# Kernel optimization log

Hardware: AMD Instinct MI355X
Metric: run time of the kernel (lower is better)

Reference implementation:

```python
import jax, jax.numpy as jnp
import numpy as np

S, B, T = 16, 32, 64        # max_sents, batch, max_tokens
V, E, H = 50000, 256, 256   # vocab, embed_size, gru_hidden (n_dim)
NC = 50                     # n_classes


def setup_inputs() -> dict:
    key = jax.random.key(0)
    ks = jax.random.split(key, 30)

    def u(k, shape, s=0.1):
        return jax.random.uniform(k, shape, minval=-s, maxval=s, dtype=jnp.float32)

    return {
        "x": jax.random.randint(ks[0], (S, B, T), 0, V, dtype=jnp.int64),
        "embed": jax.random.normal(ks[1], (V, E), dtype=jnp.float32) * 0.1,
        # word-level bi-GRU (input E, hidden H); gate order r,z,n as in torch
        "wg_Wih_f": u(ks[2], (3 * H, E)), "wg_Whh_f": u(ks[3], (3 * H, H)),
        "wg_bih_f": u(ks[4], (3 * H,)),   "wg_bhh_f": u(ks[5], (3 * H,)),
        "wg_Wih_b": u(ks[6], (3 * H, E)), "wg_Whh_b": u(ks[7], (3 * H, H)),
        "wg_bih_b": u(ks[8], (3 * H,)),   "wg_bhh_b": u(ks[9], (3 * H,)),
        "word_W": u(ks[10], (2 * H, 2 * H)),
        "word_b": u(ks[11], (2 * H, 1)),
        "word_proj": u(ks[12], (2 * H, 1)),
        # sentence-level bi-GRU (input 2H, hidden H)
        "sg_Wih_f": u(ks[13], (3 * H, 2 * H)), "sg_Whh_f": u(ks[14], (3 * H, H)),
        "sg_bih_f": u(ks[15], (3 * H,)),       "sg_bhh_f": u(ks[16], (3 * H,)),
        "sg_Wih_b": u(ks[17], (3 * H, 2 * H)), "sg_Whh_b": u(ks[18], (3 * H, H)),
        "sg_bih_b": u(ks[19], (3 * H,)),       "sg_bhh_b": u(ks[20], (3 * H,)),
        "sent_W": u(ks[21], (2 * H, 2 * H)),
        "sent_b": u(ks[22], (2 * H, 1)),
        "sent_proj": u(ks[23], (2 * H, 1)),
        "fin_W": u(ks[24], (NC, 2 * H)),
        "fin_b": u(ks[25], (NC,)),
        "state_word": jnp.zeros((2, B, H), dtype=jnp.float32),
        "state_sent": jnp.zeros((2, B, H), dtype=jnp.float32),
    }


def _gru_dir(x, h0, Wih, Whh, bih, bhh, reverse=False):
    # x: [T, B, in]; returns hidden states [T, B, H] (in original time order)
    xp = jnp.einsum('tbe,ge->tbg', x, Wih) + bih  # precompute input projections

    def step(h, xt):
        g = h @ Whh.T + bhh
        xr, xz, xn = jnp.split(xt, 3, axis=-1)
        hr, hz, hn = jnp.split(g, 3, axis=-1)
        r = jax.nn.sigmoid(xr + hr)
        z = jax.nn.sigmoid(xz + hz)
        n = jnp.tanh(xn + r * hn)
        h = (1.0 - z) * n + z * h
        return h, h

    _, hs = jax.lax.scan(step, h0, xp, reverse=reverse)
    return hs


def _bigru(x, h0, Wf, Hf, bif, bhf, Wb, Hb, bib, bhb):
    f = _gru_dir(x, h0[0], Wf, Hf, bif, bhf, reverse=False)
    b = _gru_dir(x, h0[1], Wb, Hb, bib, bhb, reverse=True)
    return jnp.concatenate([f, b], axis=-1)  # [T, B, 2H]


def _attn_pool(out, W, b, proj):
    # out: [T, B, 2H]; batch_matmul_bias(tanh) -> batch_matmul -> softmax over T -> weighted sum
    squish = jnp.tanh(jnp.einsum('tbh,hk->tbk', out, W) + b[:, 0])  # [T,B,2H]
    scores = jnp.einsum('tbk,k->tb', squish, proj[:, 0])            # [T,B]
    a = jax.nn.softmax(scores, axis=0)                              # softmax over seq
    return jnp.einsum('tb,tbh->bh', a, out)                         # [B,2H]


def reference(x, embed,
              wg_Wih_f, wg_Whh_f, wg_bih_f, wg_bhh_f,
              wg_Wih_b, wg_Whh_b, wg_bih_b, wg_bhh_b,
              word_W, word_b, word_proj,
              sg_Wih_f, sg_Whh_f, sg_bih_f, sg_bhh_f,
              sg_Wih_b, sg_Whh_b, sg_bih_b, sg_bhh_b,
              sent_W, sent_b, sent_proj,
              fin_W, fin_b, state_word, state_sent):
    e = embed[x]                         # [S,B,T,E]
    e = jnp.transpose(e, (0, 2, 1, 3))   # [S,T,B,E] (torch code transposes per sentence)

    word_out = jax.vmap(
        lambda xs: _bigru(xs, state_word,
                          wg_Wih_f, wg_Whh_f, wg_bih_f, wg_bhh_f,
                          wg_Wih_b, wg_Whh_b, wg_bih_b, wg_bhh_b)
    )(e)                                 # [S,T,B,2H]

    s = jax.vmap(lambda o: _attn_pool(o, word_W, word_b, word_proj))(word_out)  # [S,B,2H]

    sent_out = _bigru(s, state_sent,
                      sg_Wih_f, sg_Whh_f, sg_bih_f, sg_bhh_f,
                      sg_Wih_b, sg_Whh_b, sg_bih_b, sg_bhh_b)  # [S,B,2H]
    pooled = _attn_pool(sent_out, sent_W, sent_b, sent_proj)   # [B,2H]
    return pooled @ fin_W.T + fin_b                            # [B,NC] logits
```

## Files before the change

### kernel.cpp

```cpp
#include <hip/hip_runtime.h>


typedef float  f32x4  __attribute__((ext_vector_type(4)));
typedef int    i32x4  __attribute__((ext_vector_type(4)));
typedef __bf16 bf16x8 __attribute__((ext_vector_type(8)));

#define DEVINL static __device__ __forceinline__

DEVINL unsigned short f2bf(float f) {
    __bf16 b = (__bf16)f;
    return __builtin_bit_cast(unsigned short, b);
}
DEVINL float bf2f(unsigned short u) {
    unsigned int x = ((unsigned int)u) << 16;
    return __builtin_bit_cast(float, x);
}
DEVINL float bfe16(unsigned int v, int hi) {
    return bf2f((unsigned short)(hi ? (v >> 16) : (v & 0xffffu)));
}
DEVINL float sigm(float x) { return __builtin_amdgcn_rcpf(1.f + __expf(-x)); }
DEVINL float tanh_(float x) {
    x = fminf(fmaxf(x, -20.f), 20.f);
    float e = __expf(-2.f * x);
    return (1.f - e) * __builtin_amdgcn_rcpf(1.f + e);
}
DEVINL void mfma16(f32x4& acc, i32x4 a, i32x4 b) {
    acc = __builtin_amdgcn_mfma_f32_16x16x32_bf16(
        __builtin_bit_cast(bf16x8, a), __builtin_bit_cast(bf16x8, b), acc, 0, 0, 0);
}
DEVINL f32x4 zero4() { f32x4 v = {0.f, 0.f, 0.f, 0.f}; return v; }
DEVINL i32x4 pack8f(f32x4 v0, f32x4 v1) {
    i32x4 p;
    p.x = (int)((unsigned)f2bf(v0.x) | ((unsigned)f2bf(v0.y) << 16));
    p.y = (int)((unsigned)f2bf(v0.z) | ((unsigned)f2bf(v0.w) << 16));
    p.z = (int)((unsigned)f2bf(v1.x) | ((unsigned)f2bf(v1.y) << 16));
    p.w = (int)((unsigned)f2bf(v1.z) | ((unsigned)f2bf(v1.w) << 16));
    return p;
}

#define O_WPWF    ((size_t)0)
#define O_WPWB    ((size_t)1048576)
#define O_WPSGIH  ((size_t)2097152)
#define O_WPSHHF  ((size_t)3670016)
#define O_WPSHHB  ((size_t)4063232)
#define O_WPWW    ((size_t)4456448)
#define O_WPSW    ((size_t)4980736)
#define O_BIASWF  ((size_t)5505024)
#define O_BIASWB  ((size_t)5509120)
#define O_BIHCAT  ((size_t)5513216)
#define O_WOUT    ((size_t)5519360)
#define O_SCORESW ((size_t)39073792)
#define O_SSFRAG  ((size_t)39204864)
#define O_XPSENT  ((size_t)39729152)
#define O_SOFRAG  ((size_t)42874880)
#define O_SCORESS ((size_t)43399168)
#define WS_NEED_B ((size_t)43401216)
#define O_XPW     ((size_t)43401216)
#define WS_NEED_A ((size_t)144064512)

__global__ void k_prep(const float* wihf, const float* whhf,
                       const float* wihb, const float* whhb,
                       const float* sgihf, const float* sgihb,
                       const float* sghhf, const float* sghhb,
                       const float* wordW, const float* sentW,
                       const float* bihf, const float* bhhf,
                       const float* bihb, const float* bhhb,
                       const float* sgbihf, const float* sgbihb,
                       const float* sgbhhf, const float* sgbhhb,
                       unsigned short* Wpwf, unsigned short* Wpwb,
                       unsigned short* Wpsgih,
                       unsigned short* WpshhF, unsigned short* WpshhB,
                       unsigned short* WpwW, unsigned short* WpsW,
                       float* biasWf, float* biasWb, float* bihCat)
{
    const int tid0 = blockIdx.x * blockDim.x + threadIdx.x;
    const int nth  = gridDim.x * blockDim.x;

    for (int c = tid0; c < 2 * 65536; c += nth) {
        int d = c >> 16, chunk = c & 65535;
        int lane = chunk & 63, nk = chunk >> 6;
        int kf = nk & 15, nf = nk >> 4;
        int n = nf * 16 + (lane & 15);
        int k0 = kf * 32 + (lane >> 4) * 8;
        int g4 = n >> 8, jj = n & 255;
        i32x4 p = {0, 0, 0, 0};
        const bool zero = (k0 < 256) ? (g4 == 3) : (g4 == 2);
        if (!zero) {
            const float* src;
            if (k0 < 256) {
                src = (d ? wihb : wihf) + (g4 * 256 + jj) * 256 + k0;
            } else {
                int row = (g4 == 3) ? (512 + jj) : (g4 * 256 + jj);
                src = (d ? whhb : whhf) + row * 256 + (k0 - 256);
            }
            p = pack8f(*(const f32x4*)src, *(const f32x4*)(src + 4));
        }
        *(i32x4*)((d ? Wpwb : Wpwf) + chunk * 8) = p;
    }
    for (int chunk = tid0; chunk < 98304; chunk += nth) {
        int lane = chunk & 63, nk = chunk >> 6;
        int kf = nk & 15, nf = nk >> 4;
        int n = nf * 16 + (lane & 15);
        int k0 = kf * 32 + (lane >> 4) * 8;
        const float* src = (n < 768) ? sgihf + n * 512 + k0
                                     : sgihb + (n - 768) * 512 + k0;
        *(i32x4*)(Wpsgih + chunk * 8) =
            pack8f(*(const f32x4*)src, *(const f32x4*)(src + 4));
    }
    for (int c = tid0; c < 2 * 24576; c += nth) {
        int d = c >= 24576, chunk = d ? c - 24576 : c;
        int lane = chunk & 63, nk = chunk >> 6;
        int kf = nk & 7, nf = nk >> 3;
        int n = nf * 16 + (lane & 15);
        int k0 = kf * 32 + (lane >> 4) * 8;
        const float* src = (d ? sghhb : sghhf) + n * 256 + k0;
        *(i32x4*)((d ? WpshhB : WpshhF) + chunk * 8) =
            pack8f(*(const f32x4*)src, *(const f32x4*)(src + 4));
    }
    for (int c = tid0; c < 2 * 32768; c += nth) {
        int d = c >> 15, chunk = c & 32767;
        int lane = chunk & 63, nk = chunk >> 6;
        int kf = nk & 15, nf = nk >> 4;
        int n = nf * 16 + (lane & 15);
        int k0 = kf * 32 + (lane >> 4) * 8;
        const float* W = (d ? sentW : wordW) + (size_t)k0 * 512 + n;
        unsigned short us[8];
#pragma unroll
        for (int j = 0; j < 8; ++j) us[j] = f2bf(W[j * 512]);
        i32x4 p;
        p.x = (int)((unsigned)us[0] | ((unsigned)us[1] << 16));
        p.y = (int)((unsigned)us[2] | ((unsigned)us[3] << 16));
        p.z = (int)((unsigned)us[4] | ((unsigned)us[5] << 16));
        p.w = (int)((unsigned)us[6] | ((unsigned)us[7] << 16));
        *(i32x4*)((d ? WpsW : WpwW) + chunk * 8) = p;
    }
    for (int idx = tid0; idx < 2048; idx += nth) {
        int d = idx >> 10, i = idx & 1023;
        int g4 = i >> 8, j = i & 255;
        const float* bi = d ? bihb : bihf;
        const float* bh = d ? bhhb : bhhf;
        float v = (g4 == 0) ? bi[j] + bh[j]
                : (g4 == 1) ? bi[256 + j] + bh[256 + j]
                : (g4 == 2) ? bi[512 + j] : bh[512 + j];
        (d ? biasWb : biasWf)[i] = v;
    }
    for (int idx = tid0; idx < 1536; idx += nth) {
        int d = idx >= 768, j = d ? idx - 768 : idx;
        const float* bi = d ? sgbihb : sgbihf;
        const float* bh = d ? sgbhhb : sgbhhf;
        bihCat[idx] = bi[j] + ((j < 512) ? bh[j] : 0.f);
    }
}

__global__ __launch_bounds__(512, 2)
void k_xpw(const int* xg, const float* embed,
           const unsigned short* Wpwf_u, const unsigned short* Wpwb_u,
           const float* biasWf, const float* biasWb, unsigned short* xpw)
{
    __shared__ unsigned short Ebuf[2][16][256];
    const int tid = threadIdx.x, lane = tid & 63, w = tid >> 6;
    const int cid = blockIdx.x;
    const int tq = cid & 3, bh = (cid >> 2) & 1, dir = (cid >> 3) & 1, s = cid >> 4;
    const int t0 = tq * 16;
    const i32x4* Wp = (const i32x4*)(dir ? Wpwb_u : Wpwf_u);
    const float* biasW = dir ? biasWb : biasWf;
    const int b = lane & 15, rsub = lane >> 4;

    i32x4 A[3][2][8];
#pragma unroll
    for (int g = 0; g < 3; ++g)
#pragma unroll
        for (int q = 0; q < 2; ++q)
#pragma unroll
            for (int kk = 0; kk < 8; ++kk)
                A[g][q][kk] = Wp[((g * 16 + w * 2 + q) * 16 + kk) * 64 + lane];

    unsigned int biasp[3][2][2];
#pragma unroll
    for (int g = 0; g < 3; ++g)
#pragma unroll
        for (int q = 0; q < 2; ++q) {
            const int j0 = g * 256 + (w * 2 + q) * 16 + rsub * 4;
            biasp[g][q][0] = (unsigned)f2bf(biasW[j0]) |
                             ((unsigned)f2bf(biasW[j0 + 1]) << 16);
            biasp[g][q][1] = (unsigned)f2bf(biasW[j0 + 2]) |
                             ((unsigned)f2bf(biasW[j0 + 3]) << 16);
        }

    const int sb = tid >> 5, sc = tid & 31;
    const int tokrow = (s * 32 + bh * 16 + sb) * 64;
    const int sdst = sb * 512 + ((sc * 16) ^ ((sb & 7) << 4));

#define STAGE_E(BUF, T)                                                       \
    {                                                                         \
        const int tok = xg[tokrow + (T)];                                     \
        const f32x4* src = (const f32x4*)(embed + (size_t)tok * 256 + sc * 8);\
        *(i32x4*)((char*)&Ebuf[BUF][0][0] + sdst) = pack8f(src[0], src[1]);   \
    }

    STAGE_E(0, t0);
    const size_t chain = (size_t)((s * 2 + dir) * 2 + bh);
    char* const xpBase = (char*)xpw + chain * 1572864 +
                         (size_t)(rsub * 128 + b * 8);

    for (int tl = 0; tl < 16; ++tl) {
        __syncthreads();
        const int t = t0 + tl, cur = tl & 1, nxt = cur ^ 1;
        if (tl < 15) STAGE_E(nxt, t + 1);

        f32x4 acc[3][2];
#pragma unroll
        for (int g = 0; g < 3; ++g) { acc[g][0] = zero4(); acc[g][1] = zero4(); }
#pragma unroll
        for (int kk = 0; kk < 8; ++kk) {
            const int roff = b * 512 + ((kk * 64 + rsub * 16) ^ ((b & 7) << 4));
            i32x4 eb = *(const i32x4*)((const char*)&Ebuf[cur][0][0] + roff);
            mfma16(acc[0][0], A[0][0][kk], eb); mfma16(acc[0][1], A[0][1][kk], eb);
            mfma16(acc[1][0], A[1][0][kk], eb); mfma16(acc[1][1], A[1][1][kk], eb);
            mfma16(acc[2][0], A[2][0][kk], eb); mfma16(acc[2][1], A[2][1][kk], eb);
        }
        char* ob = xpBase + (size_t)t * 24576;
#pragma unroll
        for (int g = 0; g < 3; ++g)
#pragma unroll
            for (int q = 0; q < 2; ++q) {
                unsigned short us[4];
#pragma unroll
                for (int i = 0; i < 4; ++i)
                    us[i] = f2bf(acc[g][q][i] + bfe16(biasp[g][q][i >> 1], i & 1));
                uint2 pk;
                pk.x = (unsigned)us[0] | ((unsigned)us[1] << 16);
                pk.y = (unsigned)us[2] | ((unsigned)us[3] << 16);
                *(uint2*)(ob + g * 8192 + (w * 2 + q) * 512) = pk;
            }
    }
#undef STAGE_E
}

__global__ __launch_bounds__(512, 2)
void k_gru_wordA(const float* stateW,
                 const unsigned short* Wpwf_u, const unsigned short* Wpwb_u,
                 const float* biasWf, const float* biasWb,
                 const unsigned short* xpw, unsigned short* wout)
{
    __shared__ unsigned short Hbuf[2][16][256];
    const int tid = threadIdx.x, lane = tid & 63, w = tid >> 6;
    const int cid = blockIdx.x, bh = cid & 1, dir = (cid >> 1) & 1, s = cid >> 2;
    const i32x4* Wp = (const i32x4*)(dir ? Wpwb_u : Wpwf_u);
    const float* biasW = dir ? biasWb : biasWf;
    const int b = lane & 15, rsub = lane >> 4;
    const int gmap[3] = {0, 1, 3};

    i32x4 A[3][2][8];
#pragma unroll
    for (int g = 0; g < 3; ++g)
#pragma unroll
        for (int q = 0; q < 2; ++q)
#pragma unroll
            for (int kk = 0; kk < 8; ++kk)
                A[g][q][kk] =
                    Wp[((gmap[g] * 16 + w * 2 + q) * 16 + 8 + kk) * 64 + lane];

    unsigned int bhnp[2][2];
    float hreg[2][4];
#pragma unroll
    for (int q = 0; q < 2; ++q) {
        const int j0 = (w * 2 + q) * 16 + rsub * 4;
        f32x4 h0 = *(const f32x4*)(stateW + dir * 8192 + (bh * 16 + b) * 256 + j0);
        bhnp[q][0] = (unsigned)f2bf(biasW[768 + j0]) |
                     ((unsigned)f2bf(biasW[768 + j0 + 1]) << 16);
        bhnp[q][1] = (unsigned)f2bf(biasW[768 + j0 + 2]) |
                     ((unsigned)f2bf(biasW[768 + j0 + 3]) << 16);
        hreg[q][0] = h0.x; hreg[q][1] = h0.y; hreg[q][2] = h0.z; hreg[q][3] = h0.w;
        uint2 pk;
        pk.x = (unsigned)f2bf(h0.x) | ((unsigned)f2bf(h0.y) << 16);
        pk.y = (unsigned)f2bf(h0.z) | ((unsigned)f2bf(h0.w) << 16);
        const int boff = b * 512 + (((w * 2 + q) * 32 + rsub * 8) ^ ((b & 7) << 4));
        *(uint2*)((char*)&Hbuf[0][0][0] + boff) = pk;
    }
    const size_t chain = (size_t)((s * 2 + dir) * 2 + bh);
    const char* const xpBase = (const char*)xpw + chain * 1572864 +
                               (size_t)(rsub * 128 + b * 8);

    uint2 xpv[3][2];
    {
        const char* xb = xpBase + (size_t)(dir ? 63 : 0) * 24576;
#pragma unroll
        for (int g = 0; g < 3; ++g)
#pragma unroll
            for (int q = 0; q < 2; ++q)
                xpv[g][q] = *(const uint2*)(xb + g * 8192 + (w * 2 + q) * 512);
    }

    for (int ti = 0; ti < 64; ++ti) {
        __syncthreads();
        const int t = dir ? 63 - ti : ti;
        const int cur = ti & 1, nxt = cur ^ 1;

        uint2 xpn[3][2];
        if (ti < 63) {
            const char* xb = xpBase + (size_t)(dir ? t - 1 : t + 1) * 24576;
#pragma unroll
            for (int g = 0; g < 3; ++g)
#pragma unroll
                for (int q = 0; q < 2; ++q)
                    xpn[g][q] = *(const uint2*)(xb + g * 8192 + (w * 2 + q) * 512);
        }

        f32x4 acc[3][2];
#pragma unroll
        for (int g = 0; g < 3; ++g) { acc[g][0] = zero4(); acc[g][1] = zero4(); }
#pragma unroll
        for (int kk = 0; kk < 8; ++kk) {
            const int roff = b * 512 + ((kk * 64 + rsub * 16) ^ ((b & 7) << 4));
            i32x4 hb = *(const i32x4*)((const char*)&Hbuf[cur][0][0] + roff);
            mfma16(acc[0][0], A[0][0][kk], hb); mfma16(acc[0][1], A[0][1][kk], hb);
            mfma16(acc[1][0], A[1][0][kk], hb); mfma16(acc[1][1], A[1][1][kk], hb);
            mfma16(acc[2][0], A[2][0][kk], hb); mfma16(acc[2][1], A[2][1][kk], hb);
        }
        const int r = (s * 64 + t) * 32 + bh * 16 + b;
#pragma unroll
        for (int q = 0; q < 2; ++q) {
            unsigned short us[4];
#pragma unroll
            for (int i = 0; i < 4; ++i) {
                const unsigned xr = (i < 2) ? xpv[0][q].x : xpv[0][q].y;
                const unsigned xz = (i < 2) ? xpv[1][q].x : xpv[1][q].y;
                const unsigned xn = (i < 2) ? xpv[2][q].x : xpv[2][q].y;
                float rv = sigm(bfe16(xr, i & 1) + acc[0][q][i]);
                float zv = sigm(bfe16(xz, i & 1) + acc[1][q][i]);
                float nv = tanh_(bfe16(xn, i & 1) +
                                 rv * (acc[2][q][i] + bfe16(bhnp[q][i >> 1], i & 1)));
                float h = nv + zv * (hreg[q][i] - nv);
                hreg[q][i] = h;
                us[i] = f2bf(h);
            }
            uint2 pk;
            pk.x = (unsigned)us[0] | ((unsigned)us[1] << 16);
            pk.y = (unsigned)us[2] | ((unsigned)us[3] << 16);
            const int boff = b * 512 + (((w * 2 + q) * 32 + rsub * 8) ^ ((b & 7) << 4));
            *(uint2*)((char*)&Hbuf[nxt][0][0] + boff) = pk;
            const int hcol = dir * 256 + (w * 2 + q) * 16 + rsub * 4;
            const int widx = (((r >> 4) * 16 + (hcol >> 5)) * 64 + (r & 15) +
                              ((hcol >> 3) & 3) * 16) * 8 + (hcol & 7);
            *(uint2*)(wout + widx) = pk;
        }
        if (ti < 63) {
#pragma unroll
            for (int g = 0; g < 3; ++g)
#pragma unroll
                for (int q = 0; q < 2; ++q)
                    xpv[g][q] = xpn[g][q];
        }
    }
}

__global__ __launch_bounds__(1024, 4)
void k_attn_score2(const unsigned short* Afrag_u, const unsigned short* Wp_u,
                   const float* wb, const float* wp, float* scores)
{
    __shared__ i32x4 Wl[2][16][64];
    const int tid = threadIdx.x, lane = tid & 63, w = tid >> 6;
    const int rblk = blockIdx.x * 16 + w;
    const i32x4* A = (const i32x4*)Afrag_u;
    const i32x4* Wg = (const i32x4*)Wp_u;

    i32x4 a[16];
#pragma unroll
    for (int kf = 0; kf < 16; ++kf) a[kf] = A[(rblk * 16 + kf) * 64 + lane];

    i32x4* wl0 = &Wl[0][0][0];
    i32x4* wl1 = &Wl[1][0][0];
    wl0[tid] = Wg[tid];

    float partial[4] = {};
    for (int nf = 0; nf < 32; ++nf) {
        __syncthreads();
        if (nf < 31) {
            i32x4* dst = (nf & 1) ? wl0 : wl1;
            dst[tid] = Wg[(nf + 1) * 1024 + tid];
        }
        const i32x4* cur = (nf & 1) ? wl1 : wl0;
        f32x4 acc0 = zero4(), acc1 = zero4();
#pragma unroll
        for (int kf = 0; kf < 16; kf += 2) {
            mfma16(acc0, a[kf],     cur[kf * 64 + lane]);
            mfma16(acc1, a[kf + 1], cur[(kf + 1) * 64 + lane]);
        }
        const int n = nf * 16 + (lane & 15);
        const float wbn = wb[n], wpn = wp[n];
#pragma unroll
        for (int i = 0; i < 4; ++i)
            partial[i] += tanh_(acc0[i] + acc1[i] + wbn) * wpn;
    }
#pragma unroll
    for (int i = 0; i < 4; ++i) {
        float v = partial[i];
        v += __shfl_xor(v, 1); v += __shfl_xor(v, 2);
        v += __shfl_xor(v, 4); v += __shfl_xor(v, 8);
        if ((lane & 15) == 0)
            scores[rblk * 16 + (lane >> 4) * 4 + i] = v;
    }
}

__global__ void k_attn_score_small(const unsigned short* Afrag_u,
                                   const unsigned short* Wp_u,
                                   const float* wb, const float* wp, float* scores)
{
    const int tid = threadIdx.x, lane = tid & 63, w = tid >> 6;
    const int rblk = blockIdx.x * 4 + w;
    const i32x4* A = (const i32x4*)Afrag_u;
    const i32x4* Wp = (const i32x4*)Wp_u;
    i32x4 a[16];
#pragma unroll
    for (int kf = 0; kf < 16; ++kf) a[kf] = A[(rblk * 16 + kf) * 64 + lane];

    float partial[4] = {};
    for (int nf = 0; nf < 32; ++nf) {
        f32x4 acc0 = zero4(), acc1 = zero4();
#pragma unroll
        for (int kf = 0; kf < 16; kf += 2) {
            mfma16(acc0, a[kf],     Wp[(nf * 16 + kf) * 64 + lane]);
            mfma16(acc1, a[kf + 1], Wp[(nf * 16 + kf + 1) * 64 + lane]);
        }
        const int n = nf * 16 + (lane & 15);
        const float wbn = wb[n], wpn = wp[n];
#pragma unroll
        for (int i = 0; i < 4; ++i)
            partial[i] += tanh_(acc0[i] + acc1[i] + wbn) * wpn;
    }
#pragma unroll
    for (int i = 0; i < 4; ++i) {
        float v = partial[i];
        v += __shfl_xor(v, 1); v += __shfl_xor(v, 2);
        v += __shfl_xor(v, 4); v += __shfl_xor(v, 8);
        if ((lane & 15) == 0)
            scores[rblk * 16 + (lane >> 4) * 4 + i] = v;
    }
}

__global__ void k_word_pool(const float* scores, const unsigned short* wout,
                            unsigned short* ssFrag)
{
    __shared__ float aL[64];
    __shared__ float part[4][64][8];
    const int tid = threadIdx.x, l = tid & 63, w = tid >> 6;
    const int bid = blockIdx.x;
    const int s = bid >> 5, b = bid & 31;
    if (w == 0) {
        float sc = scores[s * 2048 + l * 32 + b];
        float m = sc;
#pragma unroll
        for (int d = 1; d < 64; d <<= 1) m = fmaxf(m, __shfl_xor(m, d));
        float e = __expf(sc - m), sum = e;
#pragma unroll
        for (int d = 1; d < 64; d <<= 1) sum += __shfl_xor(sum, d);
        aL[l] = e * __builtin_amdgcn_rcpf(sum);
    }
    __syncthreads();

    float acc[8] = {};
    const i32x4* WO = (const i32x4*)wout;
    for (int tt = 0; tt < 16; ++tt) {
        const int t = w * 16 + tt;
        float at = aL[t];
        int cidx = ((s * 128 + t * 2 + (b >> 4)) * 16 + (l >> 2)) * 64 +
                   (b & 15) + (l & 3) * 16;
        i32x4 ch = WO[cidx];
        acc[0] += at * bf2f((unsigned short)((unsigned)ch.x & 0xffffu));
        acc[1] += at * bf2f((unsigned short)((unsigned)ch.x >> 16));
        acc[2] += at * bf2f((unsigned short)((unsigned)ch.y & 0xffffu));
        acc[3] += at * bf2f((unsigned short)((unsigned)ch.y >> 16));
        acc[4] += at * bf2f((unsigned short)((unsigned)ch.z & 0xffffu));
        acc[5] += at * bf2f((unsigned short)((unsigned)ch.z >> 16));
        acc[6] += at * bf2f((unsigned short)((unsigned)ch.w & 0xffffu));
        acc[7] += at * bf2f((unsigned short)((unsigned)ch.w >> 16));
    }
#pragma unroll
    for (int q = 0; q < 8; ++q) part[w][l][q] = acc[q];
    __syncthreads();
    if (w == 0) {
        float fin[8];
#pragma unroll
        for (int q = 0; q < 8; ++q)
            fin[q] = part[0][l][q] + part[1][l][q] + part[2][l][q] + part[3][l][q];
        i32x4 pk;
        pk.x = (int)((unsigned)f2bf(fin[0]) | ((unsigned)f2bf(fin[1]) << 16));
        pk.y = (int)((unsigned)f2bf(fin[2]) | ((unsigned)f2bf(fin[3]) << 16));
        pk.z = (int)((unsigned)f2bf(fin[4]) | ((unsigned)f2bf(fin[5]) << 16));
        pk.w = (int)((unsigned)f2bf(fin[6]) | ((unsigned)f2bf(fin[7]) << 16));
        const int r2 = s * 32 + b;
        int cidx2 = ((r2 >> 4) * 16 + (l >> 2)) * 64 + (r2 & 15) + (l & 3) * 16;
        ((i32x4*)ssFrag)[cidx2] = pk;
    }
}

__global__ void k_sgih(const unsigned short* ssFrag_u, const unsigned short* Wp_u,
                       const float* bihCat, float* xpSent)
{
    const int tid = threadIdx.x, lane = tid & 63, w = tid >> 6;
    const int rblk = blockIdx.x, ncl = blockIdx.y;
    const i32x4* A = (const i32x4*)ssFrag_u;
    const i32x4* Wp = (const i32x4*)Wp_u;
    i32x4 a[16];
#pragma unroll
    for (int kf = 0; kf < 16; ++kf) a[kf] = A[(rblk * 16 + kf) * 64 + lane];
#pragma unroll
    for (int nfl = 0; nfl < 4; ++nfl) {
        const int nfg = ncl * 16 + w * 4 + nfl;
        f32x4 acc = zero4();
#pragma unroll
        for (int kf = 0; kf < 16; ++kf)
            mfma16(acc, a[kf], Wp[(nfg * 16 + kf) * 64 + lane]);
        const int n = nfg * 16 + (lane & 15);
        const float bb = bihCat[n];
        const int dir = n >= 768, ng = n - dir * 768;
        const int g = ng >> 8, jj = ng & 255;
#pragma unroll
        for (int i = 0; i < 4; ++i) {
            int row = rblk * 16 + (lane >> 4) * 4 + i;
            int s = row >> 5, b = row & 31;
            xpSent[(((dir * 2 + (b >> 4)) * 16 + s) * 12288) +
                   (g * 256 + jj) * 16 + (b & 15)] = acc[i] + bb;
        }
    }
}

DEVINL void gload16(const void* gsrc, void* ldst) {
    __builtin_amdgcn_global_load_lds(
        (const __attribute__((address_space(1))) unsigned int*)gsrc,
        (__attribute__((address_space(3))) unsigned int*)ldst, 16, 0, 0);
}

__global__ __launch_bounds__(512)
void k_gru_sentA(const float* stateS, const unsigned short* WpF_u,
                 const unsigned short* WpB_u, const float* bhhf, const float* bhhb,
                 const float* xpSent, unsigned short* soFrag)
{
    __shared__ unsigned short Abuf[2][16][256];
    __shared__ float xpLs[2][12288];
    const int tid = threadIdx.x, lane = tid & 63, w = tid >> 6;
    const int cid = blockIdx.x, bh = cid & 1, dir = cid >> 1;
    const i32x4* Wp = (const i32x4*)(dir ? WpB_u : WpF_u);
    const float* bhh = dir ? bhhb : bhhf;

    i32x4 B[3][2][8];
#pragma unroll
    for (int g = 0; g < 3; ++g)
#pragma unroll
        for (int q = 0; q < 2; ++q)
#pragma unroll
            for (int kk = 0; kk < 8; ++kk)
                B[g][q][kk] = Wp[((g * 16 + w * 2 + q) * 8 + kk) * 64 + lane];

    float bhn[2];
    float hreg[2][4];
#pragma unroll
    for (int q = 0; q < 2; ++q) {
        const int j = (w * 2 + q) * 16 + (lane & 15);
        bhn[q] = bhh[512 + j];
#pragma unroll
        for (int i = 0; i < 4; ++i) {
            const int b = 4 * (lane >> 4) + i;
            float h0 = stateS[dir * 8192 + (bh * 16 + b) * 256 + j];
            hreg[q][i] = h0;
            int byteoff = b * 512 + ((j * 2) ^ ((b & 7) << 4));
            *(unsigned short*)((char*)&Abuf[0][0][0] + byteoff) = f2bf(h0);
        }
    }
    const size_t xbase = (size_t)((dir * 2 + bh) * 16) * 49152;
    const int sfirst = dir ? 15 : 0;
#pragma unroll
    for (int c = 0; c < 6; ++c)
        gload16((const char*)xpSent + xbase + (size_t)sfirst * 49152 +
                    ((w * 6 + c) * 64 + lane) * 16,
                (char*)&xpLs[0][0] + (w * 6 + c) * 1024);

    for (int si = 0; si < 16; ++si) {
        __syncthreads();
        const int s = dir ? 15 - si : si;
        const int cur = si & 1, nxt = cur ^ 1;
        if (si < 15) {
            const int sn = dir ? s - 1 : s + 1;
#pragma unroll
            for (int c = 0; c < 6; ++c)
                gload16((const char*)xpSent + xbase + (size_t)sn * 49152 +
                            ((w * 6 + c) * 64 + lane) * 16,
                        (char*)&xpLs[nxt][0] + (w * 6 + c) * 1024);
        }
        f32x4 acc[3][2];
#pragma unroll
        for (int g = 0; g < 3; ++g) { acc[g][0] = zero4(); acc[g][1] = zero4(); }
#pragma unroll
        for (int kk = 0; kk < 8; ++kk) {
            const int row = lane & 15;
            const int boff = (kk * 64 + (lane >> 4) * 16) ^ ((row & 7) << 4);
            i32x4 a = *(const i32x4*)((const char*)&Abuf[cur][row][0] + boff);
#pragma unroll
            for (int g = 0; g < 3; ++g) {
                mfma16(acc[g][0], a, B[g][0][kk]);
                mfma16(acc[g][1], a, B[g][1][kk]);
            }
        }
#pragma unroll
        for (int q = 0; q < 2; ++q) {
            const int j = (w * 2 + q) * 16 + (lane & 15);
            f32x4 xr = *(const f32x4*)((const char*)&xpLs[cur][0] +
                        ((0 * 256 + j) * 16 + 4 * (lane >> 4)) * 4);
            f32x4 xz = *(const f32x4*)((const char*)&xpLs[cur][0] +
                        ((1 * 256 + j) * 16 + 4 * (lane >> 4)) * 4);
            f32x4 xn = *(const f32x4*)((const char*)&xpLs[cur][0] +
                        ((2 * 256 + j) * 16 + 4 * (lane >> 4)) * 4);
#pragma unroll
            for (int i = 0; i < 4; ++i) {
                const int b = 4 * (lane >> 4) + i;
                float rv = sigm(xr[i] + acc[0][q][i]);
                float zv = sigm(xz[i] + acc[1][q][i]);
                float nv = tanh_(xn[i] + rv * (acc[2][q][i] + bhn[q]));
                float hnew = nv + zv * (hreg[q][i] - nv);
                hreg[q][i] = hnew;
                unsigned short hb = f2bf(hnew);
                int byteoff = b * 512 + ((j * 2) ^ ((b & 7) << 4));
                *(unsigned short*)((char*)&Abuf[nxt][0][0] + byteoff) = hb;
                const int r2 = s * 32 + bh * 16 + b;
                const int hcol = dir * 256 + j;
                soFrag[(((r2 >> 4) * 16 + (hcol >> 5)) * 64 + (r2 & 15) +
                        ((hcol >> 3) & 3) * 16) * 8 + (hcol & 7)] = hb;
            }
        }
    }
}

__global__ void k_sent_pool_fin(const float* scoresS, const unsigned short* soFrag,
                                const float* finW, const float* finb, float* out)
{
    __shared__ float aL[16];
    __shared__ float pooled[512];
    __shared__ float part[4][64];
    const int l = threadIdx.x;
    const int b = blockIdx.x;

    if (l < 64) {
        float sc = (l < 16) ? scoresS[l * 32 + b] : -1e30f;
        float m = sc;
#pragma unroll
        for (int d = 1; d < 16; d <<= 1) m = fmaxf(m, __shfl_xor(m, d));
        float e = (l < 16) ? __expf(sc - m) : 0.f;
        float sum = e;
#pragma unroll
        for (int d = 1; d < 16; d <<= 1) sum += __shfl_xor(sum, d);
        if (l < 16) aL[l] = e * __builtin_amdgcn_rcpf(sum);
    }
    __syncthreads();

    if (l < 64) {
        float acc[8] = {};
        const i32x4* SO = (const i32x4*)soFrag;
        for (int si = 0; si < 16; ++si) {
            float as = aL[si];
            int r2 = si * 32 + b;
            int cidx = ((r2 >> 4) * 16 + (l >> 2)) * 64 + (r2 & 15) + (l & 3) * 16;
            i32x4 ch = SO[cidx];
            acc[0] += as * bf2f((unsigned short)((unsigned)ch.x & 0xffffu));
            acc[1] += as * bf2f((unsigned short)((unsigned)ch.x >> 16));
            acc[2] += as * bf2f((unsigned short)((unsigned)ch.y & 0xffffu));
            acc[3] += as * bf2f((unsigned short)((unsigned)ch.y >> 16));
            acc[4] += as * bf2f((unsigned short)((unsigned)ch.z & 0xffffu));
            acc[5] += as * bf2f((unsigned short)((unsigned)ch.z >> 16));
            acc[6] += as * bf2f((unsigned short)((unsigned)ch.w & 0xffffu));
            acc[7] += as * bf2f((unsigned short)((unsigned)ch.w >> 16));
        }
#pragma unroll
        for (int q = 0; q < 8; ++q) pooled[l * 8 + q] = acc[q];
    }
    __syncthreads();
    {
        const int c = l & 63, kq = l >> 6;
        float v = 0.f;
        if (c < 50) {
            const float* wrow = finW + c * 512 + kq * 128;
            const float* pp = pooled + kq * 128;
            for (int k = 0; k < 128; ++k) v += pp[k] * wrow[k];
        }
        part[kq][c] = v;
    }
    __syncthreads();
    if (l < 50)
        out[b * 50 + l] = finb[l] + part[0][l] + part[1][l] + part[2][l] + part[3][l];
}

extern "C" void kernel_launch(void* const* d_in, const int* in_sizes, int n_in,
                              void* d_out, int out_size, void* d_ws, size_t ws_size,
                              hipStream_t stream)
{
    if (ws_size < WS_NEED_A) return;

    const int*   x      = (const int*)d_in[0];
    const float* embed  = (const float*)d_in[1];
    const float* wgWihF = (const float*)d_in[2];
    const float* wgWhhF = (const float*)d_in[3];
    const float* wgBihF = (const float*)d_in[4];
    const float* wgBhhF = (const float*)d_in[5];
    const float* wgWihB = (const float*)d_in[6];
    const float* wgWhhB = (const float*)d_in[7];
    const float* wgBihB = (const float*)d_in[8];
    const float* wgBhhB = (const float*)d_in[9];
    const float* wordW  = (const float*)d_in[10];
    const float* wordB  = (const float*)d_in[11];
    const float* wordP  = (const float*)d_in[12];
    const float* sgWihF = (const float*)d_in[13];
    const float* sgWhhF = (const float*)d_in[14];
    const float* sgBihF = (const float*)d_in[15];
    const float* sgBhhF = (const float*)d_in[16];
    const float* sgWihB = (const float*)d_in[17];
    const float* sgWhhB = (const float*)d_in[18];
    const float* sgBihB = (const float*)d_in[19];
    const float* sgBhhB = (const float*)d_in[20];
    const float* sentWm = (const float*)d_in[21];
    const float* sentB  = (const float*)d_in[22];
    const float* sentP  = (const float*)d_in[23];
    const float* finW   = (const float*)d_in[24];
    const float* finB   = (const float*)d_in[25];
    const float* stateW = (const float*)d_in[26];
    const float* stateS = (const float*)d_in[27];

    char* ws = (char*)d_ws;
    unsigned short* Wpwf   = (unsigned short*)(ws + O_WPWF);
    unsigned short* Wpwb   = (unsigned short*)(ws + O_WPWB);
    unsigned short* Wpsgih = (unsigned short*)(ws + O_WPSGIH);
    unsigned short* WpshhF = (unsigned short*)(ws + O_WPSHHF);
    unsigned short* WpshhB = (unsigned short*)(ws + O_WPSHHB);
    unsigned short* WpwW   = (unsigned short*)(ws + O_WPWW);
    unsigned short* WpsW   = (unsigned short*)(ws + O_WPSW);
    float* biasWf  = (float*)(ws + O_BIASWF);
    float* biasWb  = (float*)(ws + O_BIASWB);
    float* bihCat  = (float*)(ws + O_BIHCAT);
    unsigned short* wout   = (unsigned short*)(ws + O_WOUT);
    float* scoresW = (float*)(ws + O_SCORESW);
    unsigned short* ssFrag = (unsigned short*)(ws + O_SSFRAG);
    float* xpSent  = (float*)(ws + O_XPSENT);
    unsigned short* soFrag = (unsigned short*)(ws + O_SOFRAG);
    float* scoresS = (float*)(ws + O_SCORESS);
    unsigned short* xpw    = (unsigned short*)(ws + O_XPW);

    k_prep<<<512, 256, 0, stream>>>(wgWihF, wgWhhF, wgWihB, wgWhhB,
                                    sgWihF, sgWihB, sgWhhF, sgWhhB,
                                    wordW, sentWm,
                                    wgBihF, wgBhhF, wgBihB, wgBhhB,
                                    sgBihF, sgBihB, sgBhhF, sgBhhB,
                                    Wpwf, Wpwb, Wpsgih, WpshhF, WpshhB,
                                    WpwW, WpsW, biasWf, biasWb, bihCat);

    k_xpw<<<256, 512, 0, stream>>>(x, embed, Wpwf, Wpwb, biasWf, biasWb, xpw);
    k_gru_wordA<<<64, 512, 0, stream>>>(stateW, Wpwf, Wpwb, biasWf, biasWb,
                                        xpw, wout);

    k_attn_score2<<<128, 1024, 0, stream>>>(wout, WpwW, wordB, wordP, scoresW);
    k_word_pool<<<512, 256, 0, stream>>>(scoresW, wout, ssFrag);

    k_sgih<<<dim3(32, 6), 256, 0, stream>>>(ssFrag, Wpsgih, bihCat, xpSent);
    k_gru_sentA<<<4, 512, 0, stream>>>(stateS, WpshhF, WpshhB, sgBhhF, sgBhhB,
                                       xpSent, soFrag);

    k_attn_score_small<<<8, 256, 0, stream>>>(soFrag, WpsW, sentB, sentP, scoresS);
    k_sent_pool_fin<<<32, 256, 0, stream>>>(scoresS, soFrag, finW, finB,
                                            (float*)d_out);
}
```

Baseline: 471.1 us.

## Restructure word attention pooling and drop xp prefetch in word GRU

The word-pool kernel now runs 128 blocks, each handling 16 batch rows for one sentence and one quarter of the output fragment. Each thread loops over all 64 timesteps, which removes the cross-wave shared-memory reduction, and reads are contiguous fragment-indexed vectors. Separately, the word GRU no longer software-prefetches the next timestep's input projections and instead loads them at the top of each step. That lowers register pressure but exposes load latency on the serial recurrence.

Result: faster. 454.6 us (-3.5%).

```diff
diff --git a/kernel.cpp b/kernel.cpp
--- a/kernel.cpp
+++ b/kernel.cpp
@@ -282,30 +282,18 @@
     const char* const xpBase = (const char*)xpw + chain * 1572864 +
                                (size_t)(rsub * 128 + b * 8);
 
-    uint2 xpv[3][2];
-    {
-        const char* xb = xpBase + (size_t)(dir ? 63 : 0) * 24576;
-#pragma unroll
-        for (int g = 0; g < 3; ++g)
-#pragma unroll
-            for (int q = 0; q < 2; ++q)
-                xpv[g][q] = *(const uint2*)(xb + g * 8192 + (w * 2 + q) * 512);
-    }
-
     for (int ti = 0; ti < 64; ++ti) {
         __syncthreads();
         const int t = dir ? 63 - ti : ti;
         const int cur = ti & 1, nxt = cur ^ 1;
 
-        uint2 xpn[3][2];
-        if (ti < 63) {
-            const char* xb = xpBase + (size_t)(dir ? t - 1 : t + 1) * 24576;
-#pragma unroll
-            for (int g = 0; g < 3; ++g)
-#pragma unroll
-                for (int q = 0; q < 2; ++q)
-                    xpn[g][q] = *(const uint2*)(xb + g * 8192 + (w * 2 + q) * 512);
-        }
+        uint2 xpv[3][2];
+        const char* xb = xpBase + (size_t)t * 24576;
+#pragma unroll
+        for (int g = 0; g < 3; ++g)
+#pragma unroll
+            for (int q = 0; q < 2; ++q)
+                xpv[g][q] = *(const uint2*)(xb + g * 8192 + (w * 2 + q) * 512);
 
         f32x4 acc[3][2];
 #pragma unroll
@@ -345,13 +333,6 @@
                               ((hcol >> 3) & 3) * 16) * 8 + (hcol & 7);
             *(uint2*)(wout + widx) = pk;
         }
-        if (ti < 63) {
-#pragma unroll
-            for (int g = 0; g < 3; ++g)
-#pragma unroll
-                for (int q = 0; q < 2; ++q)
-                    xpv[g][q] = xpn[g][q];
-        }
     }
 }
 
@@ -442,31 +423,35 @@
 __global__ void k_word_pool(const float* scores, const unsigned short* wout,
                             unsigned short* ssFrag)
 {
-    __shared__ float aL[64];
-    __shared__ float part[4][64][8];
-    const int tid = threadIdx.x, l = tid & 63, w = tid >> 6;
-    const int bid = blockIdx.x;
-    const int s = bid >> 5, b = bid & 31;
-    if (w == 0) {
-        float sc = scores[s * 2048 + l * 32 + b];
-        float m = sc;
-#pragma unroll
-        for (int d = 1; d < 64; d <<= 1) m = fmaxf(m, __shfl_xor(m, d));
-        float e = __expf(sc - m), sum = e;
-#pragma unroll
-        for (int d = 1; d < 64; d <<= 1) sum += __shfl_xor(sum, d);
-        aL[l] = e * __builtin_amdgcn_rcpf(sum);
+    __shared__ float aL16[16][64];
+    const int tid = threadIdx.x;
+    const int cid = blockIdx.x;
+    const int oq = cid & 3, bhi = (cid >> 2) & 1, s = cid >> 3;
+    const int o = oq * 256 + tid;
+
+    if (tid < 64) {
+        const int l = tid;
+#pragma unroll 1
+        for (int bb = 0; bb < 16; ++bb) {
+            float sc = scores[s * 2048 + l * 32 + bhi * 16 + bb];
+            float m = sc;
+#pragma unroll
+            for (int d = 1; d < 64; d <<= 1) m = fmaxf(m, __shfl_xor(m, d));
+            float e = __expf(sc - m), sum = e;
+#pragma unroll
+            for (int d = 1; d < 64; d <<= 1) sum += __shfl_xor(sum, d);
+            aL16[bb][l] = e * __builtin_amdgcn_rcpf(sum);
+        }
     }
     __syncthreads();
 
+    const int b15 = o & 15;
+    const i32x4* WO = (const i32x4*)wout;
     float acc[8] = {};
-    const i32x4* WO = (const i32x4*)wout;
-    for (int tt = 0; tt < 16; ++tt) {
-        const int t = w * 16 + tt;
-        float at = aL[t];
-        int cidx = ((s * 128 + t * 2 + (b >> 4)) * 16 + (l >> 2)) * 64 +
-                   (b & 15) + (l & 3) * 16;
-        i32x4 ch = WO[cidx];
+#pragma unroll 4
+    for (int t = 0; t < 64; ++t) {
+        float at = aL16[b15][t];
+        i32x4 ch = WO[(s * 128 + t * 2 + bhi) * 1024 + o];
         acc[0] += at * bf2f((unsigned short)((unsigned)ch.x & 0xffffu));
         acc[1] += at * bf2f((unsigned short)((unsigned)ch.x >> 16));
         acc[2] += at * bf2f((unsigned short)((unsigned)ch.y & 0xffffu));
@@ -476,23 +461,12 @@
         acc[6] += at * bf2f((unsigned short)((unsigned)ch.w & 0xffffu));
         acc[7] += at * bf2f((unsigned short)((unsigned)ch.w >> 16));
     }
-#pragma unroll
-    for (int q = 0; q < 8; ++q) part[w][l][q] = acc[q];
-    __syncthreads();
-    if (w == 0) {
-        float fin[8];
-#pragma unroll
-        for (int q = 0; q < 8; ++q)
-            fin[q] = part[0][l][q] + part[1][l][q] + part[2][l][q] + part[3][l][q];
-        i32x4 pk;
-        pk.x = (int)((unsigned)f2bf(fin[0]) | ((unsigned)f2bf(fin[1]) << 16));
-        pk.y = (int)((unsigned)f2bf(fin[2]) | ((unsigned)f2bf(fin[3]) << 16));
-        pk.z = (int)((unsigned)f2bf(fin[4]) | ((unsigned)f2bf(fin[5]) << 16));
-        pk.w = (int)((unsigned)f2bf(fin[6]) | ((unsigned)f2bf(fin[7]) << 16));
-        const int r2 = s * 32 + b;
-        int cidx2 = ((r2 >> 4) * 16 + (l >> 2)) * 64 + (r2 & 15) + (l & 3) * 16;
-        ((i32x4*)ssFrag)[cidx2] = pk;
-    }
+    i32x4 pk;
+    pk.x = (int)((unsigned)f2bf(acc[0]) | ((unsigned)f2bf(acc[1]) << 16));
+    pk.y = (int)((unsigned)f2bf(acc[2]) | ((unsigned)f2bf(acc[3]) << 16));
+    pk.z = (int)((unsigned)f2bf(acc[4]) | ((unsigned)f2bf(acc[5]) << 16));
+    pk.w = (int)((unsigned)f2bf(acc[6]) | ((unsigned)f2bf(acc[7]) << 16));
+    ((i32x4*)ssFrag)[(s * 2 + bhi) * 1024 + o] = pk;
 }
 
 __global__ void k_sgih(const unsigned short* ssFrag_u, const unsigned short* Wp_u,
@@ -756,7 +730,7 @@
                                         xpw, wout);
 
     k_attn_score2<<<128, 1024, 0, stream>>>(wout, WpwW, wordB, wordP, scoresW);
-    k_word_pool<<<512, 256, 0, stream>>>(scoresW, wout, ssFrag);
+    k_word_pool<<<128, 256, 0, stream>>>(scoresW, wout, ssFrag);
 
     k_sgih<<<dim3(32, 6), 256, 0, stream>>>(ssFrag, Wpsgih, bihCat, xpSent);
     k_gru_sentA<<<4, 512, 0, stream>>>(stateS, WpshhF, WpshhB, sgBhhF, sgBhhB,
```
